# Kernel tuning notes

Measured on AMD Instinct MI355X. Metric: run time of the kernel, lower is better.

## Reference

```python
import jax, jax.numpy as jnp
import numpy as np

B, S, D, H = 4, 2048, 1024, 16
HD = D // H


def setup_inputs() -> dict:
    key = jax.random.key(0)
    k = jax.random.split(key, 5)
    scale = 0.02
    return {
        "x": jax.random.normal(k[0], (B, S, D), dtype=jnp.float32),
        "Wq": jax.random.normal(k[1], (D, D), dtype=jnp.float32) * scale,
        "Wk": jax.random.normal(k[2], (D, D), dtype=jnp.float32) * scale,
        "Wv": jax.random.normal(k[3], (D, D), dtype=jnp.float32) * scale,
        "Wo": jax.random.normal(k[4], (D, D), dtype=jnp.float32) * scale,
    }


def reference(x, Wq, Wk, Wv, Wo):
    b, s, d_in = x.shape
    h, hd = H, HD
    # projections: [b, s, h, hd] -> [b, h, s, hd]
    q = (x @ Wq).reshape(b, s, h, hd).transpose(0, 2, 1, 3)
    k = (x @ Wk).reshape(b, s, h, hd).transpose(0, 2, 1, 3)
    v = (x @ Wv).reshape(b, s, h, hd).transpose(0, 2, 1, 3)
    # attention scores [b, h, s, s] with causal mask (match original: mask BEFORE scaling)
    scores = jnp.einsum("bhqd,bhkd->bhqk", q, k)
    causal = jnp.triu(jnp.ones((s, s), dtype=bool), k=1)
    scores = jnp.where(causal, -jnp.inf, scores)
    weights = jax.nn.softmax(scores / jnp.sqrt(jnp.float32(hd)), axis=-1)
    ctx = jnp.einsum("bhqk,bhkd->bhqd", weights, v)  # [b, h, s, hd]
    ctx = ctx.transpose(0, 2, 1, 3).reshape(b, s, h * hd)
    return ctx @ Wo
```

## Files before the change

kernel.cpp:

```cpp
#include <hip/hip_runtime.h>

#define SEQ 2048
#define DMODEL 1024
#define NH 16
#define HD 64

typedef unsigned short bf16u;
typedef unsigned short u16x8 __attribute__((ext_vector_type(8)));
typedef unsigned short u16x4 __attribute__((ext_vector_type(4)));
typedef float f32x4 __attribute__((ext_vector_type(4)));

__device__ __forceinline__ unsigned short f2b(float f) {
  __bf16 h = (__bf16)f;
  return __builtin_bit_cast(unsigned short, h);
}

__device__ __forceinline__ f32x4 mfma_bf16(u16x8 a, u16x8 b, f32x4 c) {
  return __builtin_amdgcn_mfma_f32_16x16x32_bf16(a, b, c, 0, 0, 0);
}

__global__ __launch_bounds__(256) void cast_x_kernel(const float4* __restrict__ x,
                                                     u16x4* __restrict__ xb, int n4) {
  int i = blockIdx.x * blockDim.x + threadIdx.x;
  if (i < n4) {
    float4 v = x[i];
    u16x4 o;
    o[0] = f2b(v.x); o[1] = f2b(v.y); o[2] = f2b(v.z); o[3] = f2b(v.w);
    xb[i] = o;
  }
}

__global__ __launch_bounds__(256) void transpose_w_kernel(const float* __restrict__ W0,
                                                          const float* __restrict__ W1,
                                                          const float* __restrict__ W2,
                                                          const float* __restrict__ W3,
                                                          bf16u* __restrict__ T) {
  const float* W = (blockIdx.z == 0) ? W0 : (blockIdx.z == 1) ? W1
                  : (blockIdx.z == 2) ? W2 : W3;
  bf16u* Wt = T + (size_t)blockIdx.z * (DMODEL * DMODEL);
  __shared__ float tile[32][33];
  int n = blockIdx.x * 32 + threadIdx.x;
  int k0 = blockIdx.y * 32;
  for (int i = threadIdx.y; i < 32; i += 8)
    tile[i][threadIdx.x] = W[(size_t)(k0 + i) * DMODEL + n];
  __syncthreads();
  int k = k0 + threadIdx.x;
  int n0 = blockIdx.x * 32;
  for (int i = threadIdx.y; i < 32; i += 8)
    Wt[(size_t)(n0 + i) * DMODEL + k] = f2b(tile[threadIdx.x][i]);
}

__global__ __launch_bounds__(256) void gemm_qkv_kernel(const bf16u* __restrict__ A,
                                                       const bf16u* __restrict__ Wt,
                                                       bf16u* __restrict__ QKV) {
  const bf16u* Bt = Wt + (size_t)blockIdx.z * (DMODEL * DMODEL);
  bf16u* O = QKV + (size_t)blockIdx.z * ((size_t)8192 * DMODEL);
  const bool vmode = (blockIdx.z == 2);

  __shared__ __align__(16) bf16u As[128 * 40];
  __shared__ __align__(16) bf16u Bs[128 * 40];

  const int tid = threadIdx.x;
  const int lane = tid & 63, quad = lane >> 4, l15 = lane & 15;
  const int wave = tid >> 6;
  const int wrow = (wave >> 1) * 64, wcol = (wave & 1) * 64;
  const int mbase = blockIdx.y * 128, nbase = blockIdx.x * 128;
  const int sr = tid >> 2, sc = (tid & 3) * 8;
  const bf16u* Ag = A + (size_t)(mbase + sr) * DMODEL + sc;
  const bf16u* Bg = Bt + (size_t)(nbase + sr) * DMODEL + sc;

  f32x4 acc[4][4];
#pragma unroll
  for (int i = 0; i < 4; ++i)
#pragma unroll
    for (int j = 0; j < 4; ++j) acc[i][j] = (f32x4){0.f, 0.f, 0.f, 0.f};

  for (int k0 = 0; k0 < DMODEL; k0 += 32) {
    u16x8 a0 = *(const u16x8*)(Ag + k0);
    u16x8 a1 = *(const u16x8*)(Ag + (size_t)64 * DMODEL + k0);
    u16x8 b0 = *(const u16x8*)(Bg + k0);
    u16x8 b1 = *(const u16x8*)(Bg + (size_t)64 * DMODEL + k0);
    *(u16x8*)&As[sr * 40 + sc] = a0;
    *(u16x8*)&As[(sr + 64) * 40 + sc] = a1;
    *(u16x8*)&Bs[sr * 40 + sc] = b0;
    *(u16x8*)&Bs[(sr + 64) * 40 + sc] = b1;
    __syncthreads();
    u16x8 af[4], bfr[4];
#pragma unroll
    for (int i = 0; i < 4; ++i)
      af[i] = *(const u16x8*)&As[(wrow + i * 16 + l15) * 40 + quad * 8];
#pragma unroll
    for (int j = 0; j < 4; ++j)
      bfr[j] = *(const u16x8*)&Bs[(wcol + j * 16 + l15) * 40 + quad * 8];
#pragma unroll
    for (int i = 0; i < 4; ++i)
#pragma unroll
      for (int j = 0; j < 4; ++j)
        acc[i][j] = mfma_bf16(af[i], bfr[j], acc[i][j]);
    __syncthreads();
  }

#pragma unroll
  for (int i = 0; i < 4; ++i) {
    const int mrow = mbase + wrow + i * 16 + quad * 4;
#pragma unroll
    for (int j = 0; j < 4; ++j) {
      const int n = nbase + wcol + j * 16 + l15;
      const int h = n >> 6, hd = n & 63;
#pragma unroll
      for (int r = 0; r < 4; ++r) {
        const int m = mrow + r;
        const int bb = m >> 11, ss = m & 2047;
        const size_t off = vmode
            ? (((size_t)(bb * NH + h)) * HD + hd) * SEQ + ss
            : (((size_t)(bb * NH + h)) * SEQ + ss) * HD + hd;
        O[off] = f2b(acc[i][j][r]);
      }
    }
  }
}

__global__ __launch_bounds__(256) void gemm_out_kernel(const bf16u* __restrict__ A,
                                                       const bf16u* __restrict__ Bt,
                                                       float* __restrict__ Of) {
  __shared__ __align__(16) bf16u As[128 * 40];
  __shared__ __align__(16) bf16u Bs[128 * 40];

  const int tid = threadIdx.x;
  const int lane = tid & 63, quad = lane >> 4, l15 = lane & 15;
  const int wave = tid >> 6;
  const int wrow = (wave >> 1) * 64, wcol = (wave & 1) * 64;
  const int mbase = blockIdx.y * 128, nbase = blockIdx.x * 128;
  const int sr = tid >> 2, sc = (tid & 3) * 8;
  const bf16u* Ag = A + (size_t)(mbase + sr) * DMODEL + sc;
  const bf16u* Bg = Bt + (size_t)(nbase + sr) * DMODEL + sc;

  f32x4 acc[4][4];
#pragma unroll
  for (int i = 0; i < 4; ++i)
#pragma unroll
    for (int j = 0; j < 4; ++j) acc[i][j] = (f32x4){0.f, 0.f, 0.f, 0.f};

  for (int k0 = 0; k0 < DMODEL; k0 += 32) {
    u16x8 a0 = *(const u16x8*)(Ag + k0);
    u16x8 a1 = *(const u16x8*)(Ag + (size_t)64 * DMODEL + k0);
    u16x8 b0 = *(const u16x8*)(Bg + k0);
    u16x8 b1 = *(const u16x8*)(Bg + (size_t)64 * DMODEL + k0);
    *(u16x8*)&As[sr * 40 + sc] = a0;
    *(u16x8*)&As[(sr + 64) * 40 + sc] = a1;
    *(u16x8*)&Bs[sr * 40 + sc] = b0;
    *(u16x8*)&Bs[(sr + 64) * 40 + sc] = b1;
    __syncthreads();
    u16x8 af[4], bfr[4];
#pragma unroll
    for (int i = 0; i < 4; ++i)
      af[i] = *(const u16x8*)&As[(wrow + i * 16 + l15) * 40 + quad * 8];
#pragma unroll
    for (int j = 0; j < 4; ++j)
      bfr[j] = *(const u16x8*)&Bs[(wcol + j * 16 + l15) * 40 + quad * 8];
#pragma unroll
    for (int i = 0; i < 4; ++i)
#pragma unroll
      for (int j = 0; j < 4; ++j)
        acc[i][j] = mfma_bf16(af[i], bfr[j], acc[i][j]);
    __syncthreads();
  }

#pragma unroll
  for (int i = 0; i < 4; ++i) {
    const int mrow = mbase + wrow + i * 16 + quad * 4;
#pragma unroll
    for (int j = 0; j < 4; ++j) {
      const int n = nbase + wcol + j * 16 + l15;
#pragma unroll
      for (int r = 0; r < 4; ++r)
        Of[(size_t)(mrow + r) * DMODEL + n] = acc[i][j][r];
    }
  }
}

__global__ __launch_bounds__(256, 2) void attn_kernel(const bf16u* __restrict__ Q,
                                                      const bf16u* __restrict__ K,
                                                      const bf16u* __restrict__ Vt,
                                                      bf16u* __restrict__ ctx) {
  const int bh = blockIdx.y;
  const int b = bh >> 4, h = bh & 15;
  const int bp = blockIdx.x;
  const size_t base = (size_t)bh * SEQ * HD;
  const bf16u* Qb = Q + base;
  const bf16u* Kb = K + base;
  const bf16u* Vb = Vt + base;

  const int tid = threadIdx.x;
  const int wave = tid >> 6, lane = tid & 63, quad = lane >> 4, l15 = lane & 15;

  __shared__ __align__(16) bf16u Ks[64 * 72];
  __shared__ __align__(16) bf16u Vs[64 * 72];
  __shared__ __align__(16) bf16u Ps[4][32 * 68];

  const int srow = tid >> 3;
  const int scol = (tid & 7) * 8;
  const float S = 0.18033688f;

  u16x8 ones;
#pragma unroll
  for (int i = 0; i < 8; ++i) ones[i] = 0x3F80;

#pragma unroll 1
  for (int pi = 0; pi < 2; ++pi) {
    const int qt = pi ? bp : (15 - bp);
    const int qrow0 = qt * 128 + wave * 32;
    const int ntiles = 2 * qt + 2;

    u16x8 aq[2][2];
#pragma unroll
    for (int rt = 0; rt < 2; ++rt)
#pragma unroll
      for (int ch = 0; ch < 2; ++ch)
        aq[rt][ch] = *(const u16x8*)(Qb + (size_t)(qrow0 + rt * 16 + l15) * HD + ch * 32 + quad * 8);

    f32x4 acc[2][4], accl[2];
#pragma unroll
    for (int rt = 0; rt < 2; ++rt) {
#pragma unroll
      for (int nc = 0; nc < 4; ++nc) acc[rt][nc] = (f32x4){0.f, 0.f, 0.f, 0.f};
      accl[rt] = (f32x4){0.f, 0.f, 0.f, 0.f};
    }

    u16x8 kr0 = *(const u16x8*)(Kb + (size_t)srow * HD + scol);
    u16x8 kr1 = *(const u16x8*)(Kb + (size_t)(srow + 32) * HD + scol);
    u16x8 vr0 = *(const u16x8*)(Vb + (size_t)srow * SEQ + scol);
    u16x8 vr1 = *(const u16x8*)(Vb + (size_t)(srow + 32) * SEQ + scol);

#pragma unroll 1
    for (int kt = 0; kt < ntiles; ++kt) {
      const int kbase = kt * 64;
      __syncthreads();
      *(u16x8*)&Ks[srow * 72 + scol] = kr0;
      *(u16x8*)&Ks[(srow + 32) * 72 + scol] = kr1;
      *(u16x8*)&Vs[srow * 72 + scol] = vr0;
      *(u16x8*)&Vs[(srow + 32) * 72 + scol] = vr1;
      __syncthreads();
      if (kt + 1 < ntiles) {
        const int nb = kbase + 64;
        kr0 = *(const u16x8*)(Kb + (size_t)(nb + srow) * HD + scol);
        kr1 = *(const u16x8*)(Kb + (size_t)(nb + srow + 32) * HD + scol);
        vr0 = *(const u16x8*)(Vb + (size_t)srow * SEQ + nb + scol);
        vr1 = *(const u16x8*)(Vb + (size_t)(srow + 32) * SEQ + nb + scol);
      }
      if (kbase > qrow0 + 31) continue;

      f32x4 sc[2][4];
#pragma unroll
      for (int ct = 0; ct < 4; ++ct) {
        u16x8 bk0 = *(const u16x8*)&Ks[(ct * 16 + l15) * 72 + quad * 8];
        u16x8 bk1 = *(const u16x8*)&Ks[(ct * 16 + l15) * 72 + 32 + quad * 8];
#pragma unroll
        for (int rt = 0; rt < 2; ++rt) {
          f32x4 z = {0.f, 0.f, 0.f, 0.f};
          z = mfma_bf16(aq[rt][0], bk0, z);
          z = mfma_bf16(aq[rt][1], bk1, z);
          sc[rt][ct] = z;
        }
      }

      const bool needmask = (kbase + 63 > qrow0);
#pragma unroll
      for (int rt = 0; rt < 2; ++rt) {
#pragma unroll
        for (int r = 0; r < 4; ++r) {
          const int row = qrow0 + rt * 16 + quad * 4 + r;
          float e0 = exp2f(sc[rt][0][r] * S);
          float e1 = exp2f(sc[rt][1][r] * S);
          float e2 = exp2f(sc[rt][2][r] * S);
          float e3 = exp2f(sc[rt][3][r] * S);
          if (needmask) {
            if (kbase + l15 > row) e0 = 0.f;
            if (kbase + 16 + l15 > row) e1 = 0.f;
            if (kbase + 32 + l15 > row) e2 = 0.f;
            if (kbase + 48 + l15 > row) e3 = 0.f;
          }
          const int prow = (rt * 16 + quad * 4 + r) * 68;
          Ps[wave][prow + l15] = f2b(e0);
          Ps[wave][prow + 16 + l15] = f2b(e1);
          Ps[wave][prow + 32 + l15] = f2b(e2);
          Ps[wave][prow + 48 + l15] = f2b(e3);
        }
      }

      u16x8 pa[2][2];
#pragma unroll
      for (int rt = 0; rt < 2; ++rt)
#pragma unroll
        for (int ch = 0; ch < 2; ++ch)
          pa[rt][ch] = *(const u16x8*)&Ps[wave][(rt * 16 + l15) * 68 + ch * 32 + quad * 8];

#pragma unroll
      for (int nc = 0; nc < 4; ++nc) {
        u16x8 bv0 = *(const u16x8*)&Vs[(nc * 16 + l15) * 72 + quad * 8];
        u16x8 bv1 = *(const u16x8*)&Vs[(nc * 16 + l15) * 72 + 32 + quad * 8];
#pragma unroll
        for (int rt = 0; rt < 2; ++rt) {
          acc[rt][nc] = mfma_bf16(pa[rt][0], bv0, acc[rt][nc]);
          acc[rt][nc] = mfma_bf16(pa[rt][1], bv1, acc[rt][nc]);
        }
      }
#pragma unroll
      for (int rt = 0; rt < 2; ++rt) {
        accl[rt] = mfma_bf16(pa[rt][0], ones, accl[rt]);
        accl[rt] = mfma_bf16(pa[rt][1], ones, accl[rt]);
      }
    }

#pragma unroll
    for (int rt = 0; rt < 2; ++rt) {
#pragma unroll
      for (int r = 0; r < 4; ++r) {
        const float inv = 1.0f / accl[rt][r];
        const int row = qrow0 + rt * 16 + quad * 4 + r;
        const size_t o = ((size_t)b * SEQ + row) * DMODEL + h * HD;
#pragma unroll
        for (int nc = 0; nc < 4; ++nc)
          ctx[o + nc * 16 + l15] = f2b(acc[rt][nc][r] * inv);
      }
    }
  }
}

extern "C" void kernel_launch(void* const* d_in, const int* in_sizes, int n_in,
                              void* d_out, int out_size, void* d_ws, size_t ws_size,
                              hipStream_t stream) {
  const float* x  = (const float*)d_in[0];
  const float* Wq = (const float*)d_in[1];
  const float* Wk = (const float*)d_in[2];
  const float* Wv = (const float*)d_in[3];
  const float* Wo = (const float*)d_in[4];
  float* out = (float*)d_out;

  char* ws = (char*)d_ws;
  const size_t MK = (size_t)8192 * DMODEL;
  const size_t WW = (size_t)DMODEL * DMODEL;
  bf16u* xb  = (bf16u*)ws;
  bf16u* Wt  = (bf16u*)(ws + MK * 2);
  bf16u* QKV = (bf16u*)(ws + MK * 2 + 4 * WW * 2);
  bf16u* Cx  = (bf16u*)(ws + MK * 2 + 4 * WW * 2 + 3 * MK * 2);

  const int n4 = (int)(MK / 4);
  cast_x_kernel<<<dim3(n4 / 256), 256, 0, stream>>>((const float4*)x, (u16x4*)xb, n4);
  transpose_w_kernel<<<dim3(32, 32, 4), dim3(32, 8), 0, stream>>>(Wq, Wk, Wv, Wo, Wt);
  gemm_qkv_kernel<<<dim3(8, 64, 3), 256, 0, stream>>>(xb, Wt, QKV);
  attn_kernel<<<dim3(8, 64), 256, 0, stream>>>(QKV, QKV + MK, QKV + 2 * MK, Cx);
  gemm_out_kernel<<<dim3(8, 64), 256, 0, stream>>>(Cx, Wt + 3 * WW, out);
}
```

Before: 304.8 us.

## Load GEMM tiles straight to LDS with XOR-swizzled layout, vectorize V stores

Both projection GEMMs now fill shared memory with global_load_lds, which copies global data directly into LDS without staging it in registers. The unpadded 32-column tiles use an XOR swizzle on the 16-byte chunk index to avoid bank conflicts. The V-transposed epilogue packs four bf16 values into a single vector store instead of four scalar stores. The aim is lower register pressure and fewer load instructions, but the loop is still single-buffered with two barriers per K step, so load latency is not hidden.

```diff
diff --git a/kernel.cpp b/kernel.cpp
--- a/kernel.cpp
+++ b/kernel.cpp
@@ -17,6 +17,12 @@
 
 __device__ __forceinline__ f32x4 mfma_bf16(u16x8 a, u16x8 b, f32x4 c) {
   return __builtin_amdgcn_mfma_f32_16x16x32_bf16(a, b, c, 0, 0, 0);
+}
+
+__device__ __forceinline__ void load16_lds(const bf16u* g, bf16u* l) {
+  __builtin_amdgcn_global_load_lds(
+      (const __attribute__((address_space(1))) unsigned int*)(const void*)g,
+      (__attribute__((address_space(3))) unsigned int*)(void*)l, 16, 0, 0);
 }
 
 __global__ __launch_bounds__(256) void cast_x_kernel(const float4* __restrict__ x,
@@ -50,6 +56,7 @@
     Wt[(size_t)(n0 + i) * DMODEL + k] = f2b(tile[threadIdx.x][i]);
 }
 
+
 __global__ __launch_bounds__(256) void gemm_qkv_kernel(const bf16u* __restrict__ A,
                                                        const bf16u* __restrict__ Wt,
                                                        bf16u* __restrict__ QKV) {
@@ -57,17 +64,27 @@
   bf16u* O = QKV + (size_t)blockIdx.z * ((size_t)8192 * DMODEL);
   const bool vmode = (blockIdx.z == 2);
 
-  __shared__ __align__(16) bf16u As[128 * 40];
-  __shared__ __align__(16) bf16u Bs[128 * 40];
+  __shared__ __align__(16) bf16u As[128 * 32];
+  __shared__ __align__(16) bf16u Bs[128 * 32];
 
   const int tid = threadIdx.x;
   const int lane = tid & 63, quad = lane >> 4, l15 = lane & 15;
   const int wave = tid >> 6;
   const int wrow = (wave >> 1) * 64, wcol = (wave & 1) * 64;
   const int mbase = blockIdx.y * 128, nbase = blockIdx.x * 128;
-  const int sr = tid >> 2, sc = (tid & 3) * 8;
-  const bf16u* Ag = A + (size_t)(mbase + sr) * DMODEL + sc;
-  const bf16u* Bg = Bt + (size_t)(nbase + sr) * DMODEL + sc;
+
+  const int r0 = tid >> 2, s0 = tid & 3;
+  const int g0 = s0 ^ (r0 & 3);
+  const bf16u* Ag0 = A + (size_t)(mbase + r0) * DMODEL + g0 * 8;
+  const bf16u* Bg0 = Bt + (size_t)(nbase + r0) * DMODEL + g0 * 8;
+  const bf16u* Ag1 = Ag0 + (size_t)64 * DMODEL;
+  const bf16u* Bg1 = Bg0 + (size_t)64 * DMODEL;
+  bf16u* Al0 = &As[tid * 8];
+  bf16u* Al1 = &As[2048 + tid * 8];
+  bf16u* Bl0 = &Bs[tid * 8];
+  bf16u* Bl1 = &Bs[2048 + tid * 8];
+
+  const int xq = (quad ^ (l15 & 3)) * 8;
 
   f32x4 acc[4][4];
 #pragma unroll
@@ -76,45 +93,43 @@
     for (int j = 0; j < 4; ++j) acc[i][j] = (f32x4){0.f, 0.f, 0.f, 0.f};
 
   for (int k0 = 0; k0 < DMODEL; k0 += 32) {
-    u16x8 a0 = *(const u16x8*)(Ag + k0);
-    u16x8 a1 = *(const u16x8*)(Ag + (size_t)64 * DMODEL + k0);
-    u16x8 b0 = *(const u16x8*)(Bg + k0);
-    u16x8 b1 = *(const u16x8*)(Bg + (size_t)64 * DMODEL + k0);
-    *(u16x8*)&As[sr * 40 + sc] = a0;
-    *(u16x8*)&As[(sr + 64) * 40 + sc] = a1;
-    *(u16x8*)&Bs[sr * 40 + sc] = b0;
-    *(u16x8*)&Bs[(sr + 64) * 40 + sc] = b1;
+    __syncthreads();
+    load16_lds(Ag0 + k0, Al0);
+    load16_lds(Ag1 + k0, Al1);
+    load16_lds(Bg0 + k0, Bl0);
+    load16_lds(Bg1 + k0, Bl1);
     __syncthreads();
     u16x8 af[4], bfr[4];
 #pragma unroll
     for (int i = 0; i < 4; ++i)
-      af[i] = *(const u16x8*)&As[(wrow + i * 16 + l15) * 40 + quad * 8];
+      af[i] = *(const u16x8*)&As[(wrow + i * 16 + l15) * 32 + xq];
 #pragma unroll
     for (int j = 0; j < 4; ++j)
-      bfr[j] = *(const u16x8*)&Bs[(wcol + j * 16 + l15) * 40 + quad * 8];
+      bfr[j] = *(const u16x8*)&Bs[(wcol + j * 16 + l15) * 32 + xq];
 #pragma unroll
     for (int i = 0; i < 4; ++i)
 #pragma unroll
       for (int j = 0; j < 4; ++j)
         acc[i][j] = mfma_bf16(af[i], bfr[j], acc[i][j]);
-    __syncthreads();
   }
 
 #pragma unroll
   for (int i = 0; i < 4; ++i) {
     const int mrow = mbase + wrow + i * 16 + quad * 4;
+    const int bb = mrow >> 11, ss = mrow & 2047;
 #pragma unroll
     for (int j = 0; j < 4; ++j) {
       const int n = nbase + wcol + j * 16 + l15;
       const int h = n >> 6, hd = n & 63;
-#pragma unroll
-      for (int r = 0; r < 4; ++r) {
-        const int m = mrow + r;
-        const int bb = m >> 11, ss = m & 2047;
-        const size_t off = vmode
-            ? (((size_t)(bb * NH + h)) * HD + hd) * SEQ + ss
-            : (((size_t)(bb * NH + h)) * SEQ + ss) * HD + hd;
-        O[off] = f2b(acc[i][j][r]);
+      if (vmode) {
+        u16x4 pk;
+#pragma unroll
+        for (int r = 0; r < 4; ++r) pk[r] = f2b(acc[i][j][r]);
+        *(u16x4*)&O[(((size_t)(bb * NH + h)) * HD + hd) * SEQ + ss] = pk;
+      } else {
+#pragma unroll
+        for (int r = 0; r < 4; ++r)
+          O[(((size_t)(bb * NH + h)) * SEQ + ss + r) * HD + hd] = f2b(acc[i][j][r]);
       }
     }
   }
@@ -123,17 +138,27 @@
 __global__ __launch_bounds__(256) void gemm_out_kernel(const bf16u* __restrict__ A,
                                                        const bf16u* __restrict__ Bt,
                                                        float* __restrict__ Of) {
-  __shared__ __align__(16) bf16u As[128 * 40];
-  __shared__ __align__(16) bf16u Bs[128 * 40];
+  __shared__ __align__(16) bf16u As[128 * 32];
+  __shared__ __align__(16) bf16u Bs[128 * 32];
 
   const int tid = threadIdx.x;
   const int lane = tid & 63, quad = lane >> 4, l15 = lane & 15;
   const int wave = tid >> 6;
   const int wrow = (wave >> 1) * 64, wcol = (wave & 1) * 64;
   const int mbase = blockIdx.y * 128, nbase = blockIdx.x * 128;
-  const int sr = tid >> 2, sc = (tid & 3) * 8;
-  const bf16u* Ag = A + (size_t)(mbase + sr) * DMODEL + sc;
-  const bf16u* Bg = Bt + (size_t)(nbase + sr) * DMODEL + sc;
+
+  const int r0 = tid >> 2, s0 = tid & 3;
+  const int g0 = s0 ^ (r0 & 3);
+  const bf16u* Ag0 = A + (size_t)(mbase + r0) * DMODEL + g0 * 8;
+  const bf16u* Bg0 = Bt + (size_t)(nbase + r0) * DMODEL + g0 * 8;
+  const bf16u* Ag1 = Ag0 + (size_t)64 * DMODEL;
+  const bf16u* Bg1 = Bg0 + (size_t)64 * DMODEL;
+  bf16u* Al0 = &As[tid * 8];
+  bf16u* Al1 = &As[2048 + tid * 8];
+  bf16u* Bl0 = &Bs[tid * 8];
+  bf16u* Bl1 = &Bs[2048 + tid * 8];
+
+  const int xq = (quad ^ (l15 & 3)) * 8;
 
   f32x4 acc[4][4];
 #pragma unroll
@@ -142,28 +167,24 @@
     for (int j = 0; j < 4; ++j) acc[i][j] = (f32x4){0.f, 0.f, 0.f, 0.f};
 
   for (int k0 = 0; k0 < DMODEL; k0 += 32) {
-    u16x8 a0 = *(const u16x8*)(Ag + k0);
-    u16x8 a1 = *(const u16x8*)(Ag + (size_t)64 * DMODEL + k0);
-    u16x8 b0 = *(const u16x8*)(Bg + k0);
-    u16x8 b1 = *(const u16x8*)(Bg + (size_t)64 * DMODEL + k0);
-    *(u16x8*)&As[sr * 40 + sc] = a0;
-    *(u16x8*)&As[(sr + 64) * 40 + sc] = a1;
-    *(u16x8*)&Bs[sr * 40 + sc] = b0;
-    *(u16x8*)&Bs[(sr + 64) * 40 + sc] = b1;
+    __syncthreads();
+    load16_lds(Ag0 + k0, Al0);
+    load16_lds(Ag1 + k0, Al1);
+    load16_lds(Bg0 + k0, Bl0);
+    load16_lds(Bg1 + k0, Bl1);
     __syncthreads();
     u16x8 af[4], bfr[4];
 #pragma unroll
     for (int i = 0; i < 4; ++i)
-      af[i] = *(const u16x8*)&As[(wrow + i * 16 + l15) * 40 + quad * 8];
+      af[i] = *(const u16x8*)&As[(wrow + i * 16 + l15) * 32 + xq];
 #pragma unroll
     for (int j = 0; j < 4; ++j)
-      bfr[j] = *(const u16x8*)&Bs[(wcol + j * 16 + l15) * 40 + quad * 8];
+      bfr[j] = *(const u16x8*)&Bs[(wcol + j * 16 + l15) * 32 + xq];
 #pragma unroll
     for (int i = 0; i < 4; ++i)
 #pragma unroll
       for (int j = 0; j < 4; ++j)
         acc[i][j] = mfma_bf16(af[i], bfr[j], acc[i][j]);
-    __syncthreads();
   }
 
 #pragma unroll
```

After: 280.8 us. 7.9% less time.
